# Kernel optimization log

Measured on AMD Instinct MI355X. Metric: run time of the kernel, lower is better.

Reference implementation:

```python
import jax, jax.numpy as jnp
import numpy as np

B = 8192
DIMS = [5, 1024, 1024, 512, 512, 512, 512, 2]  # model_param
L1, L2, OBS_X, OBS_Y, R = 3.0, 3.0, 0.0, 7.0, 4.0


def _linear_params(key, fan_in, fan_out):
    kw, kb = jax.random.split(key)
    lim = 1.0 / np.sqrt(fan_in)
    W = jax.random.uniform(kw, (fan_in, fan_out), jnp.float32, -lim, lim)
    b = jax.random.uniform(kb, (fan_out,), jnp.float32, -lim, lim)
    return W, b


def setup_inputs() -> dict:
    key = jax.random.key(0)
    keys = jax.random.split(key, 9)
    x = jax.random.normal(keys[0], (B, DIMS[0]), jnp.float32)
    W1, b1 = _linear_params(keys[1], DIMS[0], DIMS[1])
    W2, b2 = _linear_params(keys[2], DIMS[1], DIMS[2])
    W31, b31 = _linear_params(keys[3], DIMS[2], DIMS[3])
    W32, b32 = _linear_params(keys[4], DIMS[2], DIMS[4])
    W41, b41 = _linear_params(keys[5], DIMS[3], DIMS[5])
    W42, b42 = _linear_params(keys[6], DIMS[4], DIMS[6])
    W51, b51 = _linear_params(keys[7], DIMS[5], DIMS[7])
    W52, b52 = _linear_params(keys[8], DIMS[6], DIMS[7])
    return {
        'x': x, 'sgn': 1,
        'mean': jnp.zeros((DIMS[0],), jnp.float32),
        'std': jnp.ones((DIMS[0],), jnp.float32),
        'mean_label': jnp.zeros((2,), jnp.float32),
        'std_label': jnp.ones((2,), jnp.float32),
        'W1': W1, 'b1': b1, 'W2': W2, 'b2': b2,
        'W31': W31, 'b31': b31, 'W32': W32, 'b32': b32,
        'W41': W41, 'b41': b41, 'W42': W42, 'b42': b42,
        'W51': W51, 'b51': b51, 'W52': W52, 'b52': b52,
    }


def _forward(x, mean, std, mean_label, std_label,
             W1, b1, W2, b2, W31, b31, W32, b32,
             W41, b41, W42, b42, W51, b51, W52, b52):
    act = jax.nn.relu
    x0 = x * std + mean                      # un-normalized state [B,5]
    x1 = act(x @ W1 + b1)
    x2 = act(x1 @ W2 + b2)
    x31 = act(x2 @ W31 + b31)
    x32 = act(x2 @ W32 + b32)
    x41 = act(x31 @ W41 + b41)
    x42 = act(x32 @ W42 + b42)
    x51 = x41 @ W51 + b51                    # QP linear term p  [B,2]
    x52 = 4.0 * jax.nn.sigmoid(x42 @ W52 + b52)  # CBF class-K gains [B,2]

    # dCBF terms (two-link arm obstacle barrier)
    t1, w1, t2, w2 = x0[:, 0], x0[:, 1], x0[:, 2], x0[:, 3]
    s1, s2, c1, c2 = jnp.sin(t1), jnp.sin(t2), jnp.cos(t1), jnp.cos(t2)
    px = L1 * c1 + L2 * c2 - OBS_X
    py = L1 * s1 + L2 * s2 - OBS_Y
    vx = -L1 * s1 * w1 - L2 * s2 * w2
    vy = L1 * c1 * w1 + L2 * c2 * w2
    barrier = px * px + py * py - R * R
    b_dot = 2.0 * (px * vx + py * vy)
    Lf2b = (2.0 * (vx * vx + vy * vy)
            + 2.0 * px * (-L1 * c1 * w1 * w1 - L2 * c2 * w2 * w2)
            + 2.0 * py * (-L1 * s1 * w1 * w1 - L2 * s2 * w2 * w2))
    # G (single inequality row, 2 columns), G u <= h
    G1 = -(2.0 * px * (-L1 * s1) + 2.0 * py * (L1 * c1))
    G2 = -(2.0 * px * (-L2 * s2) + 2.0 * py * (L2 * c2))
    G = jnp.stack([G1, G2], axis=1)          # [B,2]
    h = Lf2b + (x52[:, 0] + x52[:, 1]) * b_dot + x52[:, 0] * x52[:, 1] * barrier  # [B]

    # QP: min 0.5||u||^2 + x51.u  s.t. G u <= h  -> closed-form KKT projection
    u0 = -x51                                 # unconstrained optimum
    viol = jnp.sum(G * u0, axis=1) - h        # [B]
    lam = jnp.maximum(viol, 0.0) / (jnp.sum(G * G, axis=1) + 1e-12)
    u = u0 - lam[:, None] * G                 # [B,2]
    return (u - mean_label) / std_label


def reference(x, sgn, mean, std, mean_label, std_label,
              W1, b1, W2, b2, W31, b31, W32, b32,
              W41, b41, W42, b42, W51, b51, W52, b52):
    # sgn == 1 -> batched QP branch (the trained/deployed path)
    return _forward(x, mean, std, mean_label, std_label,
                    W1, b1, W2, b2, W31, b31, W32, b32,
                    W41, b41, W42, b42, W51, b51, W52, b52)
```

## Files before the change

kernel.cpp:

```cpp
#include <hip/hip_runtime.h>
#include <hip/hip_bf16.h>
#include <math.h>


typedef __attribute__((ext_vector_type(4))) float f32x4;
typedef __attribute__((ext_vector_type(8))) short bf16x8;

static __device__ __forceinline__ unsigned short f2bf(float f) {
    unsigned int u = __float_as_uint(f);
    unsigned int r = (u + 0x7fffu + ((u >> 16) & 1u)) >> 16;
    return (unsigned short)r;
}
static __device__ __forceinline__ float bf2f(unsigned short h) {
    return __uint_as_float(((unsigned int)h) << 16);
}

#define TBM 128
#define TBN 256
#define TBK 64

#define GLL(gp, lp) __builtin_amdgcn_global_load_lds( \
    (const __attribute__((address_space(1))) void*)(gp), \
    (__attribute__((address_space(3))) void*)(lp), 16, 0, 0)

#define VMC(N)  asm volatile("s_waitcnt vmcnt(" #N ")" ::: "memory")
#define BAR()   __builtin_amdgcn_s_barrier()
#define SB0()   __builtin_amdgcn_sched_barrier(0)

__device__ __forceinline__ void gemm_core(
    const unsigned short* __restrict__ A, int lda,
    const unsigned short* __restrict__ Bt, int ldb,
    const float* __restrict__ bias,
    unsigned short* __restrict__ C, int ldc,
    int K, int m0, int n0b, int c0)
{
    __shared__ __align__(16) short sA[3][TBM * TBK];
    __shared__ __align__(16) short sB[3][TBN * TBK];

    const int tid  = threadIdx.x;
    const int w    = tid >> 6;
    const int lane = tid & 63;

    const int srow = lane >> 3;
    const int skq  = (lane & 7) ^ ((lane >> 3) & 7);
    const unsigned short* aP0 =
        A + (size_t)(m0 + 16 * w + srow) * lda + skq * 8;
    const unsigned short* aP1 = aP0 + 8 * lda;
    const unsigned short* bP0 =
        Bt + (size_t)(n0b + 32 * w + srow) * ldb + skq * 8;
    const unsigned short* bP1 = bP0 + 8 * ldb;
    const unsigned short* bP2 = bP0 + 16 * ldb;
    const unsigned short* bP3 = bP0 + 24 * ldb;

    const int wrow = (w >> 2) * 64;
    const int wcol = (w & 3) * 64;
    const int fr = lane & 15;
    const int fq = lane >> 4;
    const int swz0 = ((fq)     ^ (fr & 7)) * 8;
    const int swz1 = ((4 + fq) ^ (fr & 7)) * 8;

    f32x4 acc[4][4] = {};
    const int nt = K / TBK;

    auto STAGE = [&](int kt, int b) {
        const size_t ko = (size_t)kt * TBK;
        short* la = &sA[b][0];
        short* lb = &sB[b][0];
        GLL(aP0 + ko, la + (2 * w)     * 512);
        GLL(aP1 + ko, la + (2 * w + 1) * 512);
        GLL(bP0 + ko, lb + (4 * w)     * 512);
        GLL(bP1 + ko, lb + (4 * w + 1) * 512);
        GLL(bP2 + ko, lb + (4 * w + 2) * 512);
        GLL(bP3 + ko, lb + (4 * w + 3) * 512);
    };

    STAGE(0, 0);
    STAGE(1, 1);
    VMC(6);
    BAR();
    SB0();

    int cur = 0, stg = 2;
    for (int t = 0; t < nt; ++t) {
        const short* sAp = &sA[cur][0];
        const short* sBp = &sB[cur][0];

        bf16x8 af[2][4], bf[2][4];
        #pragma unroll
        for (int m = 0; m < 4; ++m) {
            const int r = (wrow + m * 16 + fr) * 64;
            af[0][m] = *reinterpret_cast<const bf16x8*>(&sAp[r + swz0]);
            af[1][m] = *reinterpret_cast<const bf16x8*>(&sAp[r + swz1]);
        }
        #pragma unroll
        for (int n = 0; n < 4; ++n) {
            const int r = (wcol + n * 16 + fr) * 64;
            bf[0][n] = *reinterpret_cast<const bf16x8*>(&sBp[r + swz0]);
            bf[1][n] = *reinterpret_cast<const bf16x8*>(&sBp[r + swz1]);
        }

        if (t + 2 < nt) STAGE(t + 2, stg);

        __builtin_amdgcn_s_setprio(1);
        #pragma unroll
        for (int kh = 0; kh < 2; ++kh)
            #pragma unroll
            for (int m = 0; m < 4; ++m)
                #pragma unroll
                for (int n = 0; n < 4; ++n)
                    acc[m][n] = __builtin_amdgcn_mfma_f32_16x16x32_bf16(
                        af[kh][m], bf[kh][n], acc[m][n], 0, 0, 0);
        __builtin_amdgcn_s_setprio(0);

        if (t + 1 < nt) {
            if (t + 2 < nt) { VMC(6); } else { VMC(0); }
            BAR();
            SB0();
        }
        cur = (cur == 2) ? 0 : cur + 1;
        stg = (stg == 2) ? 0 : stg + 1;
    }

    #pragma unroll
    for (int n = 0; n < 4; ++n) {
        const int cl = wcol + n * 16 + fr;
        const float bv = bias[n0b + cl];
        #pragma unroll
        for (int m = 0; m < 4; ++m) {
            const int rbase = m0 + wrow + m * 16 + fq * 4;
            #pragma unroll
            for (int r = 0; r < 4; ++r) {
                float v = fmaxf(acc[m][n][r] + bv, 0.0f);
                C[(size_t)(rbase + r) * ldc + c0 + cl] = f2bf(v);
            }
        }
    }
}

static __device__ __forceinline__ int xcd_sid() {
    const int bid = blockIdx.y * gridDim.x + blockIdx.x;
    return (bid & 7) * 32 + (bid >> 3);
}

__global__ __launch_bounds__(512, 2) void gemm_bf16(
    const unsigned short* __restrict__ A, int lda,
    const unsigned short* __restrict__ Bt, int ldb,
    const float* __restrict__ bias,
    unsigned short* __restrict__ C, int ldc, int K)
{
    const int sid = xcd_sid();
    const int n0 = (sid & 3) * TBN;
    const int m0 = (sid >> 2) * TBM;
    gemm_core(A, lda, Bt, ldb, bias, C, ldc, K, m0, n0, n0);
}

__global__ __launch_bounds__(512, 2) void gemm_bf16_l4(
    const unsigned short* __restrict__ x3,
    const unsigned short* __restrict__ W41t,
    const unsigned short* __restrict__ W42t,
    const float* __restrict__ b41, const float* __restrict__ b42,
    unsigned short* __restrict__ x4)
{
    const int sid = xcd_sid();
    const int xp  = sid & 3;
    const int g   = xp >> 1;
    const int n0b = (xp & 1) * TBN;
    const int m0  = (sid >> 2) * TBM;
    const unsigned short* A  = x3 + (g ? 512 : 0);
    const unsigned short* Bt = g ? W42t : W41t;
    const float* bias        = g ? b42 : b41;
    gemm_core(A, 1024, Bt, 512, bias, x4, 1024, 512, m0, n0b, g * 512 + n0b);
}

__global__ __launch_bounds__(256) void prep_weights(
    const float* __restrict__ W2,  const float* __restrict__ W31,
    const float* __restrict__ W32, const float* __restrict__ W41,
    const float* __restrict__ W42, const float* __restrict__ b31,
    const float* __restrict__ b32,
    const float* __restrict__ x,   const float* __restrict__ W1,
    const float* __restrict__ b1,
    unsigned short* __restrict__ W2t,  unsigned short* __restrict__ W3t,
    unsigned short* __restrict__ W41t, unsigned short* __restrict__ W42t,
    float* __restrict__ b3c, unsigned short* __restrict__ xb1)
{
    const int z = blockIdx.z;
    if (z == 6) {
        const int r0 = (blockIdx.y * 32 + blockIdx.x) * 8;
        const int j4 = threadIdx.x * 4;
        float4 wv[5];
        #pragma unroll
        for (int k = 0; k < 5; ++k)
            wv[k] = *reinterpret_cast<const float4*>(&W1[k * 1024 + j4]);
        const float4 bb = *reinterpret_cast<const float4*>(&b1[j4]);
        #pragma unroll
        for (int r = 0; r < 8; ++r) {
            const float* xr = &x[(size_t)(r0 + r) * 5];
            float4 acc = bb;
            #pragma unroll
            for (int k = 0; k < 5; ++k) {
                const float xv = xr[k];
                acc.x = fmaf(xv, wv[k].x, acc.x);
                acc.y = fmaf(xv, wv[k].y, acc.y);
                acc.z = fmaf(xv, wv[k].z, acc.z);
                acc.w = fmaf(xv, wv[k].w, acc.w);
            }
            ushort4 o;
            o.x = f2bf(fmaxf(acc.x, 0.f));
            o.y = f2bf(fmaxf(acc.y, 0.f));
            o.z = f2bf(fmaxf(acc.z, 0.f));
            o.w = f2bf(fmaxf(acc.w, 0.f));
            *reinterpret_cast<ushort4*>(&xb1[(size_t)(r0 + r) * 1024 + j4]) = o;
        }
        return;
    }
    if (z == 5) {
        if (blockIdx.x == 0 && blockIdx.y == 0) {
            for (int i = threadIdx.x; i < 1024; i += 256)
                b3c[i] = (i < 512) ? b31[i] : b32[i - 512];
        }
        return;
    }
    const float* src; unsigned short* dst; int K, N;
    switch (z) {
        case 0:  src = W2;  dst = W2t;              K = 1024; N = 1024; break;
        case 1:  src = W31; dst = W3t;              K = 1024; N = 512;  break;
        case 2:  src = W32; dst = W3t + 512 * 1024; K = 1024; N = 512;  break;
        case 3:  src = W41; dst = W41t;             K = 512;  N = 512;  break;
        default: src = W42; dst = W42t;             K = 512;  N = 512;  break;
    }
    const int k0 = blockIdx.x * 32, n0 = blockIdx.y * 32;
    if (k0 >= K || n0 >= N) return;

    __shared__ float t[32][33];
    const int tx = threadIdx.x & 31, ty = threadIdx.x >> 5;
    #pragma unroll
    for (int i = 0; i < 32; i += 8)
        t[ty + i][tx] = src[(size_t)(k0 + ty + i) * N + n0 + tx];
    __syncthreads();
    #pragma unroll
    for (int i = 0; i < 32; i += 8)
        dst[(size_t)(n0 + ty + i) * K + k0 + tx] = f2bf(t[tx][ty + i]);
}

__global__ __launch_bounds__(256) void head_kernel(
    const unsigned short* __restrict__ x4,
    const float* __restrict__ W51, const float* __restrict__ b51,
    const float* __restrict__ W52, const float* __restrict__ b52,
    const float* __restrict__ x,   const float* __restrict__ mean,
    const float* __restrict__ stdv, const float* __restrict__ mean_label,
    const float* __restrict__ std_label, float* __restrict__ out)
{
    const int wave = threadIdx.x >> 6;
    const int lane = threadIdx.x & 63;
    const int row = blockIdx.x * 4 + wave;

    const unsigned short* p41 = x4 + (size_t)row * 1024;
    const bf16x8 v1 = *reinterpret_cast<const bf16x8*>(p41 + lane * 8);
    const bf16x8 v2 = *reinterpret_cast<const bf16x8*>(p41 + 512 + lane * 8);
    const float4 q0 = *reinterpret_cast<const float4*>(W51 + lane * 16 + 0);
    const float4 q1 = *reinterpret_cast<const float4*>(W51 + lane * 16 + 4);
    const float4 q2 = *reinterpret_cast<const float4*>(W51 + lane * 16 + 8);
    const float4 q3 = *reinterpret_cast<const float4*>(W51 + lane * 16 + 12);
    const float4 s0 = *reinterpret_cast<const float4*>(W52 + lane * 16 + 0);
    const float4 s1 = *reinterpret_cast<const float4*>(W52 + lane * 16 + 4);
    const float4 s2 = *reinterpret_cast<const float4*>(W52 + lane * 16 + 8);
    const float4 s3 = *reinterpret_cast<const float4*>(W52 + lane * 16 + 12);

    float a0, a1, a2, a3;
    {
        const float e0 = bf2f((unsigned short)v1[0]), e1 = bf2f((unsigned short)v1[1]),
                    e2 = bf2f((unsigned short)v1[2]), e3 = bf2f((unsigned short)v1[3]),
                    e4 = bf2f((unsigned short)v1[4]), e5 = bf2f((unsigned short)v1[5]),
                    e6 = bf2f((unsigned short)v1[6]), e7 = bf2f((unsigned short)v1[7]);
        a0 = e0*q0.x + e1*q0.z + e2*q1.x + e3*q1.z + e4*q2.x + e5*q2.z + e6*q3.x + e7*q3.z;
        a1 = e0*q0.y + e1*q0.w + e2*q1.y + e3*q1.w + e4*q2.y + e5*q2.w + e6*q3.y + e7*q3.w;
        const float f0 = bf2f((unsigned short)v2[0]), f1 = bf2f((unsigned short)v2[1]),
                    f2 = bf2f((unsigned short)v2[2]), f3 = bf2f((unsigned short)v2[3]),
                    f4 = bf2f((unsigned short)v2[4]), f5 = bf2f((unsigned short)v2[5]),
                    f6 = bf2f((unsigned short)v2[6]), f7 = bf2f((unsigned short)v2[7]);
        a2 = f0*s0.x + f1*s0.z + f2*s1.x + f3*s1.z + f4*s2.x + f5*s2.z + f6*s3.x + f7*s3.z;
        a3 = f0*s0.y + f1*s0.w + f2*s1.y + f3*s1.w + f4*s2.y + f5*s2.w + f6*s3.y + f7*s3.w;
    }
    #pragma unroll
    for (int off = 32; off >= 1; off >>= 1) {
        a0 += __shfl_down(a0, off);
        a1 += __shfl_down(a1, off);
        a2 += __shfl_down(a2, off);
        a3 += __shfl_down(a3, off);
    }

    if (lane == 0) {
        const float L1c = 3.0f, L2c = 3.0f, OBSX = 0.0f, OBSY = 7.0f, Rc = 4.0f;
        const float t1 = x[row * 5 + 0] * stdv[0] + mean[0];
        const float w1 = x[row * 5 + 1] * stdv[1] + mean[1];
        const float t2 = x[row * 5 + 2] * stdv[2] + mean[2];
        const float w2 = x[row * 5 + 3] * stdv[3] + mean[3];
        const float s1v = sinf(t1), c1 = cosf(t1);
        const float s2v = sinf(t2), c2 = cosf(t2);
        const float px = L1c * c1 + L2c * c2 - OBSX;
        const float py = L1c * s1v + L2c * s2v - OBSY;
        const float vx = -L1c * s1v * w1 - L2c * s2v * w2;
        const float vy =  L1c * c1 * w1 + L2c * c2 * w2;
        const float barrier = px * px + py * py - Rc * Rc;
        const float b_dot = 2.0f * (px * vx + py * vy);
        const float Lf2b = 2.0f * (vx * vx + vy * vy)
                         + 2.0f * px * (-L1c * c1 * w1 * w1 - L2c * c2 * w2 * w2)
                         + 2.0f * py * (-L1c * s1v * w1 * w1 - L2c * s2v * w2 * w2);
        const float G1 = -(2.0f * px * (-L1c * s1v) + 2.0f * py * (L1c * c1));
        const float G2 = -(2.0f * px * (-L2c * s2v) + 2.0f * py * (L2c * c2));

        const float x51_0 = a0 + b51[0];
        const float x51_1 = a1 + b51[1];
        const float z0 = a2 + b52[0];
        const float z1 = a3 + b52[1];
        const float x52_0 = 4.0f / (1.0f + expf(-z0));
        const float x52_1 = 4.0f / (1.0f + expf(-z1));

        const float u0_0 = -x51_0;
        const float u0_1 = -x51_1;
        const float h = Lf2b + (x52_0 + x52_1) * b_dot + x52_0 * x52_1 * barrier;
        const float viol = G1 * u0_0 + G2 * u0_1 - h;
        const float lam = fmaxf(viol, 0.0f) / (G1 * G1 + G2 * G2 + 1e-12f);
        const float u_0 = u0_0 - lam * G1;
        const float u_1 = u0_1 - lam * G2;
        out[row * 2 + 0] = (u_0 - mean_label[0]) / std_label[0];
        out[row * 2 + 1] = (u_1 - mean_label[1]) / std_label[1];
    }
}

extern "C" void kernel_launch(void* const* d_in, const int* in_sizes, int n_in,
                              void* d_out, int out_size, void* d_ws, size_t ws_size,
                              hipStream_t stream) {
    const float* x          = (const float*)d_in[0];
    const float* mean       = (const float*)d_in[2];
    const float* stdv       = (const float*)d_in[3];
    const float* mean_label = (const float*)d_in[4];
    const float* std_label  = (const float*)d_in[5];
    const float* W1  = (const float*)d_in[6];   const float* b1  = (const float*)d_in[7];
    const float* W2  = (const float*)d_in[8];   const float* b2  = (const float*)d_in[9];
    const float* W31 = (const float*)d_in[10];  const float* b31 = (const float*)d_in[11];
    const float* W32 = (const float*)d_in[12];  const float* b32 = (const float*)d_in[13];
    const float* W41 = (const float*)d_in[14];  const float* b41 = (const float*)d_in[15];
    const float* W42 = (const float*)d_in[16];  const float* b42 = (const float*)d_in[17];
    const float* W51 = (const float*)d_in[18];  const float* b51 = (const float*)d_in[19];
    const float* W52 = (const float*)d_in[20];  const float* b52 = (const float*)d_in[21];
    float* out = (float*)d_out;

    char* ws = (char*)d_ws;
    const size_t MiB = 1024 * 1024;
    unsigned short* xb1  = (unsigned short*)(ws + 0);
    unsigned short* x2b  = (unsigned short*)(ws + 16 * MiB);
    unsigned short* x3   = xb1;
    unsigned short* x4   = x2b;
    unsigned short* W2t  = (unsigned short*)(ws + 32 * MiB);
    unsigned short* W3t  = (unsigned short*)(ws + 34 * MiB);
    unsigned short* W41t = (unsigned short*)(ws + 36 * MiB);
    unsigned short* W42t = (unsigned short*)(ws + 36 * MiB + 512 * 1024);
    float*          b3c  = (float*)(ws + 37 * MiB);

    prep_weights<<<dim3(32, 32, 7), 256, 0, stream>>>(
        W2, W31, W32, W41, W42, b31, b32, x, W1, b1,
        W2t, W3t, W41t, W42t, b3c, xb1);

    dim3 gBig(1024 / TBN, 8192 / TBM);
    gemm_bf16<<<gBig, 512, 0, stream>>>(xb1, 1024, W2t, 1024, b2, x2b, 1024, 1024);
    gemm_bf16<<<gBig, 512, 0, stream>>>(x2b, 1024, W3t, 1024, b3c, x3, 1024, 1024);

    gemm_bf16_l4<<<dim3(4, 64), 512, 0, stream>>>(x3, W41t, W42t, b41, b42, x4);

    head_kernel<<<2048, 256, 0, stream>>>(x4, W51, b51, W52, b52,
                                          x, mean, stdv, mean_label, std_label, out);
}
```

Measured before the change: 78.95 us.

## Split GEMM k-tile into four phased LDS-read/MFMA clusters with interleaved prefetch

Restructures the main loop so each k-tile runs in four phases. Each phase loads a few A/B fragments from LDS, issues one slice of the next-next global-to-LDS prefetch, then runs eight MFMAs under raised priority, with barriers between phases. The aim is to interleave LDS reads, global loads and MFMA work across waves in a ping-pong style and to cut register pressure from fragment arrays. It adds many extra workgroup barriers per tile, which could stall waves.

New measurement: 90.95 us. 1.15x slower.

```diff
diff --git a/kernel.cpp b/kernel.cpp
--- a/kernel.cpp
+++ b/kernel.cpp
@@ -24,8 +24,23 @@
     (__attribute__((address_space(3))) void*)(lp), 16, 0, 0)
 
 #define VMC(N)  asm volatile("s_waitcnt vmcnt(" #N ")" ::: "memory")
+#define LGKM0() asm volatile("s_waitcnt lgkmcnt(0)" ::: "memory")
 #define BAR()   __builtin_amdgcn_s_barrier()
 #define SB0()   __builtin_amdgcn_sched_barrier(0)
+#define PRIO1() __builtin_amdgcn_s_setprio(1)
+#define PRIO0() __builtin_amdgcn_s_setprio(0)
+
+#define MFMA_PAIR(AF0, AF1, M0, M1)                                          \
+    do {                                                                     \
+        acc[M0][0] = __builtin_amdgcn_mfma_f32_16x16x32_bf16(AF0, bf[0], acc[M0][0], 0, 0, 0); \
+        acc[M0][1] = __builtin_amdgcn_mfma_f32_16x16x32_bf16(AF0, bf[1], acc[M0][1], 0, 0, 0); \
+        acc[M0][2] = __builtin_amdgcn_mfma_f32_16x16x32_bf16(AF0, bf[2], acc[M0][2], 0, 0, 0); \
+        acc[M0][3] = __builtin_amdgcn_mfma_f32_16x16x32_bf16(AF0, bf[3], acc[M0][3], 0, 0, 0); \
+        acc[M1][0] = __builtin_amdgcn_mfma_f32_16x16x32_bf16(AF1, bf[0], acc[M1][0], 0, 0, 0); \
+        acc[M1][1] = __builtin_amdgcn_mfma_f32_16x16x32_bf16(AF1, bf[1], acc[M1][1], 0, 0, 0); \
+        acc[M1][2] = __builtin_amdgcn_mfma_f32_16x16x32_bf16(AF1, bf[2], acc[M1][2], 0, 0, 0); \
+        acc[M1][3] = __builtin_amdgcn_mfma_f32_16x16x32_bf16(AF1, bf[3], acc[M1][3], 0, 0, 0); \
+    } while (0)
 
 __device__ __forceinline__ void gemm_core(
     const unsigned short* __restrict__ A, int lda,
@@ -62,20 +77,27 @@
     f32x4 acc[4][4] = {};
     const int nt = K / TBK;
 
-    auto STAGE = [&](int kt, int b) {
+    auto STAGE_A = [&](int kt, int b) {
         const size_t ko = (size_t)kt * TBK;
         short* la = &sA[b][0];
-        short* lb = &sB[b][0];
         GLL(aP0 + ko, la + (2 * w)     * 512);
         GLL(aP1 + ko, la + (2 * w + 1) * 512);
+    };
+    auto STAGE_B01 = [&](int kt, int b) {
+        const size_t ko = (size_t)kt * TBK;
+        short* lb = &sB[b][0];
         GLL(bP0 + ko, lb + (4 * w)     * 512);
         GLL(bP1 + ko, lb + (4 * w + 1) * 512);
+    };
+    auto STAGE_B23 = [&](int kt, int b) {
+        const size_t ko = (size_t)kt * TBK;
+        short* lb = &sB[b][0];
         GLL(bP2 + ko, lb + (4 * w + 2) * 512);
         GLL(bP3 + ko, lb + (4 * w + 3) * 512);
     };
 
-    STAGE(0, 0);
-    STAGE(1, 1);
+    STAGE_A(0, 0); STAGE_B01(0, 0); STAGE_B23(0, 0);
+    STAGE_A(1, 1); STAGE_B01(1, 1); STAGE_B23(1, 1);
     VMC(6);
     BAR();
     SB0();
@@ -84,36 +106,44 @@
     for (int t = 0; t < nt; ++t) {
         const short* sAp = &sA[cur][0];
         const short* sBp = &sB[cur][0];
-
-        bf16x8 af[2][4], bf[2][4];
-        #pragma unroll
-        for (int m = 0; m < 4; ++m) {
-            const int r = (wrow + m * 16 + fr) * 64;
-            af[0][m] = *reinterpret_cast<const bf16x8*>(&sAp[r + swz0]);
-            af[1][m] = *reinterpret_cast<const bf16x8*>(&sAp[r + swz1]);
-        }
-        #pragma unroll
-        for (int n = 0; n < 4; ++n) {
-            const int r = (wcol + n * 16 + fr) * 64;
-            bf[0][n] = *reinterpret_cast<const bf16x8*>(&sBp[r + swz0]);
-            bf[1][n] = *reinterpret_cast<const bf16x8*>(&sBp[r + swz1]);
-        }
-
-        if (t + 2 < nt) STAGE(t + 2, stg);
-
-        __builtin_amdgcn_s_setprio(1);
-        #pragma unroll
-        for (int kh = 0; kh < 2; ++kh)
-            #pragma unroll
-            for (int m = 0; m < 4; ++m)
-                #pragma unroll
-                for (int n = 0; n < 4; ++n)
-                    acc[m][n] = __builtin_amdgcn_mfma_f32_16x16x32_bf16(
-                        af[kh][m], bf[kh][n], acc[m][n], 0, 0, 0);
-        __builtin_amdgcn_s_setprio(0);
-
+        const bool st = (t + 2 < nt);
+        bf16x8 bf[4], a0, a1;
+
+        bf[0] = *reinterpret_cast<const bf16x8*>(&sBp[(wcol +  0 + fr) * 64 + swz0]);
+        bf[1] = *reinterpret_cast<const bf16x8*>(&sBp[(wcol + 16 + fr) * 64 + swz0]);
+        bf[2] = *reinterpret_cast<const bf16x8*>(&sBp[(wcol + 32 + fr) * 64 + swz0]);
+        bf[3] = *reinterpret_cast<const bf16x8*>(&sBp[(wcol + 48 + fr) * 64 + swz0]);
+        a0 = *reinterpret_cast<const bf16x8*>(&sAp[(wrow +  0 + fr) * 64 + swz0]);
+        a1 = *reinterpret_cast<const bf16x8*>(&sAp[(wrow + 16 + fr) * 64 + swz0]);
+        if (st) STAGE_A(t + 2, stg);
+        BAR(); LGKM0(); SB0();
+        PRIO1(); MFMA_PAIR(a0, a1, 0, 1); PRIO0();
+        BAR();
+
+        a0 = *reinterpret_cast<const bf16x8*>(&sAp[(wrow + 32 + fr) * 64 + swz0]);
+        a1 = *reinterpret_cast<const bf16x8*>(&sAp[(wrow + 48 + fr) * 64 + swz0]);
+        if (st) STAGE_B01(t + 2, stg);
+        BAR(); LGKM0(); SB0();
+        PRIO1(); MFMA_PAIR(a0, a1, 2, 3); PRIO0();
+        BAR();
+
+        bf[0] = *reinterpret_cast<const bf16x8*>(&sBp[(wcol +  0 + fr) * 64 + swz1]);
+        bf[1] = *reinterpret_cast<const bf16x8*>(&sBp[(wcol + 16 + fr) * 64 + swz1]);
+        bf[2] = *reinterpret_cast<const bf16x8*>(&sBp[(wcol + 32 + fr) * 64 + swz1]);
+        bf[3] = *reinterpret_cast<const bf16x8*>(&sBp[(wcol + 48 + fr) * 64 + swz1]);
+        a0 = *reinterpret_cast<const bf16x8*>(&sAp[(wrow +  0 + fr) * 64 + swz1]);
+        a1 = *reinterpret_cast<const bf16x8*>(&sAp[(wrow + 16 + fr) * 64 + swz1]);
+        if (st) STAGE_B23(t + 2, stg);
+        BAR(); LGKM0(); SB0();
+        PRIO1(); MFMA_PAIR(a0, a1, 0, 1); PRIO0();
+        BAR();
+
+        a0 = *reinterpret_cast<const bf16x8*>(&sAp[(wrow + 32 + fr) * 64 + swz1]);
+        a1 = *reinterpret_cast<const bf16x8*>(&sAp[(wrow + 48 + fr) * 64 + swz1]);
+        BAR(); LGKM0(); SB0();
+        PRIO1(); MFMA_PAIR(a0, a1, 2, 3); PRIO0();
         if (t + 1 < nt) {
-            if (t + 2 < nt) { VMC(6); } else { VMC(0); }
+            if (st) { VMC(6); } else { VMC(0); }
             BAR();
             SB0();
         }
```

## Load GEMM A tiles directly into registers, double-buffered, bypassing LDS

Applied to the files above, without the earlier changes.

Each wave now reads its A fragments straight from global memory into registers, double-buffered as even/odd sets with the main loop unrolled by two. Only the B tile still goes through the three-stage LDS pipeline, so the waitcnt thresholds are lowered to match the smaller number of async loads. The goal is to cut LDS traffic and shared-memory footprint for A. In exchange, the four waves that share the same A rows each reload them from global memory, register pressure rises, and the unroll-by-two assumes an even K-tile count.

Result: slower. 134.8 us (+70.7%).

```diff
diff --git a/kernel.cpp b/kernel.cpp
--- a/kernel.cpp
+++ b/kernel.cpp
@@ -34,7 +34,6 @@
     unsigned short* __restrict__ C, int ldc,
     int K, int m0, int n0b, int c0)
 {
-    __shared__ __align__(16) short sA[3][TBM * TBK];
     __shared__ __align__(16) short sB[3][TBN * TBK];
 
     const int tid  = threadIdx.x;
@@ -43,9 +42,6 @@
 
     const int srow = lane >> 3;
     const int skq  = (lane & 7) ^ ((lane >> 3) & 7);
-    const unsigned short* aP0 =
-        A + (size_t)(m0 + 16 * w + srow) * lda + skq * 8;
-    const unsigned short* aP1 = aP0 + 8 * lda;
     const unsigned short* bP0 =
         Bt + (size_t)(n0b + 32 * w + srow) * ldb + skq * 8;
     const unsigned short* bP1 = bP0 + 8 * ldb;
@@ -59,67 +55,72 @@
     const int swz0 = ((fq)     ^ (fr & 7)) * 8;
     const int swz1 = ((4 + fq) ^ (fr & 7)) * 8;
 
+    const unsigned short* aRow[4];
+    #pragma unroll
+    for (int m_ = 0; m_ < 4; ++m_)
+        aRow[m_] = A + (size_t)(m0 + wrow + m_ * 16 + fr) * lda + fq * 8;
+
     f32x4 acc[4][4] = {};
+    bf16x8 aE[4][2], aO[4][2];
     const int nt = K / TBK;
 
-    auto STAGE = [&](int kt, int b) {
+#define LOAD_A(DST, KT)                                                      \
+    do {                                                                     \
+        _Pragma("unroll") for (int m_ = 0; m_ < 4; ++m_)                     \
+            _Pragma("unroll") for (int kh_ = 0; kh_ < 2; ++kh_)              \
+                DST[m_][kh_] = *reinterpret_cast<const bf16x8*>(             \
+                    aRow[m_] + (size_t)(KT) * TBK + kh_ * 32);               \
+    } while (0)
+
+    auto STAGE_B = [&](int kt, int b) {
         const size_t ko = (size_t)kt * TBK;
-        short* la = &sA[b][0];
         short* lb = &sB[b][0];
-        GLL(aP0 + ko, la + (2 * w)     * 512);
-        GLL(aP1 + ko, la + (2 * w + 1) * 512);
         GLL(bP0 + ko, lb + (4 * w)     * 512);
         GLL(bP1 + ko, lb + (4 * w + 1) * 512);
         GLL(bP2 + ko, lb + (4 * w + 2) * 512);
         GLL(bP3 + ko, lb + (4 * w + 3) * 512);
     };
 
-    STAGE(0, 0);
-    STAGE(1, 1);
-    VMC(6);
+#define GBODY(T, AUSE, ANEXT)                                                \
+    {                                                                        \
+        const short* sBp = &sB[cur][0];                                      \
+        if ((T) + 1 < nt) LOAD_A(ANEXT, (T) + 1);                \
+        if ((T) + 2 < nt) STAGE_B((T) + 2, stg);                 \
+        bf16x8 bfr[2][4];                                                    \
+        _Pragma("unroll") for (int n_ = 0; n_ < 4; ++n_) {                   \
+            const int r_ = (wcol + n_ * 16 + fr) * 64;                       \
+            bfr[0][n_] = *reinterpret_cast<const bf16x8*>(&sBp[r_ + swz0]);  \
+            bfr[1][n_] = *reinterpret_cast<const bf16x8*>(&sBp[r_ + swz1]);  \
+        }                                                                    \
+        __builtin_amdgcn_s_setprio(1);                                       \
+        _Pragma("unroll") for (int kh_ = 0; kh_ < 2; ++kh_)                  \
+            _Pragma("unroll") for (int m_ = 0; m_ < 4; ++m_)                 \
+                _Pragma("unroll") for (int n_ = 0; n_ < 4; ++n_)             \
+                    acc[m_][n_] = __builtin_amdgcn_mfma_f32_16x16x32_bf16(   \
+                        AUSE[m_][kh_], bfr[kh_][n_], acc[m_][n_], 0, 0, 0);  \
+        __builtin_amdgcn_s_setprio(0);                                       \
+        if ((T) + 1 < nt) {                                                  \
+            if ((T) + 2 < nt) { VMC(4); } else { VMC(0); }                   \
+            BAR(); SB0();                                                    \
+        }                                                                    \
+        cur = (cur == 2) ? 0 : cur + 1;                                      \
+        stg = (stg == 2) ? 0 : stg + 1;                                      \
+    }
+
+    LOAD_A(aE, 0);
+    STAGE_B(0, 0);
+    STAGE_B(1, 1);
+    VMC(4);
     BAR();
     SB0();
 
     int cur = 0, stg = 2;
-    for (int t = 0; t < nt; ++t) {
-        const short* sAp = &sA[cur][0];
-        const short* sBp = &sB[cur][0];
-
-        bf16x8 af[2][4], bf[2][4];
-        #pragma unroll
-        for (int m = 0; m < 4; ++m) {
-            const int r = (wrow + m * 16 + fr) * 64;
-            af[0][m] = *reinterpret_cast<const bf16x8*>(&sAp[r + swz0]);
-            af[1][m] = *reinterpret_cast<const bf16x8*>(&sAp[r + swz1]);
-        }
-        #pragma unroll
-        for (int n = 0; n < 4; ++n) {
-            const int r = (wcol + n * 16 + fr) * 64;
-            bf[0][n] = *reinterpret_cast<const bf16x8*>(&sBp[r + swz0]);
-            bf[1][n] = *reinterpret_cast<const bf16x8*>(&sBp[r + swz1]);
-        }
-
-        if (t + 2 < nt) STAGE(t + 2, stg);
-
-        __builtin_amdgcn_s_setprio(1);
-        #pragma unroll
-        for (int kh = 0; kh < 2; ++kh)
-            #pragma unroll
-            for (int m = 0; m < 4; ++m)
-                #pragma unroll
-                for (int n = 0; n < 4; ++n)
-                    acc[m][n] = __builtin_amdgcn_mfma_f32_16x16x32_bf16(
-                        af[kh][m], bf[kh][n], acc[m][n], 0, 0, 0);
-        __builtin_amdgcn_s_setprio(0);
-
-        if (t + 1 < nt) {
-            if (t + 2 < nt) { VMC(6); } else { VMC(0); }
-            BAR();
-            SB0();
-        }
-        cur = (cur == 2) ? 0 : cur + 1;
-        stg = (stg == 2) ? 0 : stg + 1;
-    }
+    for (int t = 0; t < nt; t += 2) {
+        GBODY(t,     aE, aO);
+        GBODY(t + 1, aO, aE);
+    }
+#undef GBODY
+#undef LOAD_A
 
     #pragma unroll
     for (int n = 0; n < 4; ++n) {
```

## Split GEMM K-tile into two phases with interleaved loads and barriers

Applied to the files above, without the earlier changes.

Each 64-wide K tile in the MFMA main loop is now split into two 32-wide halves. Each half loads its fragments from LDS, issues part of the next-next stage's global-to-LDS copies, synchronizes with barriers, then runs 16 MFMAs. The goal is to spread memory issue across the iteration and lower register pressure by holding half as many fragments at once, in the style of ping-pong scheduling. The cost is three extra workgroup barriers per iteration, which may add stalls.

Result: slower. 83.44 us (+5.7%).

```diff
diff --git a/kernel.cpp b/kernel.cpp
--- a/kernel.cpp
+++ b/kernel.cpp
@@ -24,8 +24,11 @@
     (__attribute__((address_space(3))) void*)(lp), 16, 0, 0)
 
 #define VMC(N)  asm volatile("s_waitcnt vmcnt(" #N ")" ::: "memory")
+#define LGKM0() asm volatile("s_waitcnt lgkmcnt(0)" ::: "memory")
 #define BAR()   __builtin_amdgcn_s_barrier()
 #define SB0()   __builtin_amdgcn_sched_barrier(0)
+#define PRIO1() __builtin_amdgcn_s_setprio(1)
+#define PRIO0() __builtin_amdgcn_s_setprio(0)
 
 __device__ __forceinline__ void gemm_core(
     const unsigned short* __restrict__ A, int lda,
@@ -62,20 +65,24 @@
     f32x4 acc[4][4] = {};
     const int nt = K / TBK;
 
-    auto STAGE = [&](int kt, int b) {
+    auto STAGE_P0 = [&](int kt, int b) {
         const size_t ko = (size_t)kt * TBK;
         short* la = &sA[b][0];
         short* lb = &sB[b][0];
         GLL(aP0 + ko, la + (2 * w)     * 512);
         GLL(aP1 + ko, la + (2 * w + 1) * 512);
         GLL(bP0 + ko, lb + (4 * w)     * 512);
+    };
+    auto STAGE_P1 = [&](int kt, int b) {
+        const size_t ko = (size_t)kt * TBK;
+        short* lb = &sB[b][0];
         GLL(bP1 + ko, lb + (4 * w + 1) * 512);
         GLL(bP2 + ko, lb + (4 * w + 2) * 512);
         GLL(bP3 + ko, lb + (4 * w + 3) * 512);
     };
 
-    STAGE(0, 0);
-    STAGE(1, 1);
+    STAGE_P0(0, 0); STAGE_P1(0, 0);
+    STAGE_P0(1, 1); STAGE_P1(1, 1);
     VMC(6);
     BAR();
     SB0();
@@ -84,36 +91,49 @@
     for (int t = 0; t < nt; ++t) {
         const short* sAp = &sA[cur][0];
         const short* sBp = &sB[cur][0];
-
-        bf16x8 af[2][4], bf[2][4];
-        #pragma unroll
-        for (int m = 0; m < 4; ++m) {
-            const int r = (wrow + m * 16 + fr) * 64;
-            af[0][m] = *reinterpret_cast<const bf16x8*>(&sAp[r + swz0]);
-            af[1][m] = *reinterpret_cast<const bf16x8*>(&sAp[r + swz1]);
-        }
-        #pragma unroll
-        for (int n = 0; n < 4; ++n) {
-            const int r = (wcol + n * 16 + fr) * 64;
-            bf[0][n] = *reinterpret_cast<const bf16x8*>(&sBp[r + swz0]);
-            bf[1][n] = *reinterpret_cast<const bf16x8*>(&sBp[r + swz1]);
-        }
-
-        if (t + 2 < nt) STAGE(t + 2, stg);
-
-        __builtin_amdgcn_s_setprio(1);
-        #pragma unroll
-        for (int kh = 0; kh < 2; ++kh)
+        const bool st = (t + 2 < nt);
+        bf16x8 af[4], bfr[4];
+
+        #pragma unroll
+        for (int m = 0; m < 4; ++m)
+            af[m] = *reinterpret_cast<const bf16x8*>(
+                &sAp[(wrow + m * 16 + fr) * 64 + swz0]);
+        #pragma unroll
+        for (int n = 0; n < 4; ++n)
+            bfr[n] = *reinterpret_cast<const bf16x8*>(
+                &sBp[(wcol + n * 16 + fr) * 64 + swz0]);
+        if (st) STAGE_P0(t + 2, stg);
+        BAR(); LGKM0(); SB0();
+        PRIO1();
+        #pragma unroll
+        for (int m = 0; m < 4; ++m)
             #pragma unroll
-            for (int m = 0; m < 4; ++m)
-                #pragma unroll
-                for (int n = 0; n < 4; ++n)
-                    acc[m][n] = __builtin_amdgcn_mfma_f32_16x16x32_bf16(
-                        af[kh][m], bf[kh][n], acc[m][n], 0, 0, 0);
-        __builtin_amdgcn_s_setprio(0);
-
+            for (int n = 0; n < 4; ++n)
+                acc[m][n] = __builtin_amdgcn_mfma_f32_16x16x32_bf16(
+                    af[m], bfr[n], acc[m][n], 0, 0, 0);
+        PRIO0();
+        BAR();
+
+        #pragma unroll
+        for (int m = 0; m < 4; ++m)
+            af[m] = *reinterpret_cast<const bf16x8*>(
+                &sAp[(wrow + m * 16 + fr) * 64 + swz1]);
+        #pragma unroll
+        for (int n = 0; n < 4; ++n)
+            bfr[n] = *reinterpret_cast<const bf16x8*>(
+                &sBp[(wcol + n * 16 + fr) * 64 + swz1]);
+        if (st) STAGE_P1(t + 2, stg);
+        BAR(); LGKM0(); SB0();
+        PRIO1();
+        #pragma unroll
+        for (int m = 0; m < 4; ++m)
+            #pragma unroll
+            for (int n = 0; n < 4; ++n)
+                acc[m][n] = __builtin_amdgcn_mfma_f32_16x16x32_bf16(
+                    af[m], bfr[n], acc[m][n], 0, 0, 0);
+        PRIO0();
         if (t + 1 < nt) {
-            if (t + 2 < nt) { VMC(6); } else { VMC(0); }
+            if (st) { VMC(6); } else { VMC(0); }
             BAR();
             SB0();
         }
```
